# Kernel optimization log

Hardware: AMD Instinct MI355X
Metric: run time of the kernel (lower is better)

Reference implementation:

```python
import jax, jax.numpy as jnp
import numpy as np

D_MODEL = 1024
HEADS = 16
D_HEAD = D_MODEL // HEADS


def setup_inputs() -> dict:
    key = jax.random.key(0)
    ks = jax.random.split(key, 7)
    s = 1.0 / np.sqrt(D_MODEL)
    x = jax.random.normal(ks[0], (4, 2048, D_MODEL), dtype=jnp.float32)
    Wq = jax.random.uniform(ks[1], (D_MODEL, D_MODEL), jnp.float32, -s, s)
    bq = jax.random.uniform(ks[2], (D_MODEL,), jnp.float32, -s, s)
    Wk = jax.random.uniform(ks[3], (D_MODEL, D_MODEL), jnp.float32, -s, s)
    bk = jax.random.uniform(ks[4], (D_MODEL,), jnp.float32, -s, s)
    Wv = jax.random.uniform(ks[5], (D_MODEL, D_MODEL), jnp.float32, -s, s)
    bv = jax.random.uniform(ks[6], (D_MODEL,), jnp.float32, -s, s)
    return {"x": x, "Wq": Wq, "bq": bq, "Wk": Wk, "bk": bk, "Wv": Wv, "bv": bv}


def reference(x, Wq, bq, Wk, bk, Wv, bv):
    B, S, D = x.shape
    # QKV projections, split heads: [B, H, S, Dh]
    def split(t):
        return t.reshape(B, S, HEADS, D_HEAD).transpose(0, 2, 1, 3)
    q = split(x @ Wq + bq)
    k = split(x @ Wk + bk)
    v = split(x @ Wv + bv)
    scores = jnp.einsum('bhqd,bhkd->bhqk', q, k) / np.sqrt(D_HEAD).astype(jnp.float32)
    attn = jax.nn.softmax(scores, axis=-1)
    out = jnp.einsum('bhqk,bhkd->bhqd', attn, v)
    return out.transpose(0, 2, 1, 3).reshape(B, S, D)
```

## Files before the change

### kernel.cpp

```cpp
#include <hip/hip_runtime.h>

typedef _Float16 f16;
typedef __attribute__((ext_vector_type(2))) _Float16 f16x2;
typedef __attribute__((ext_vector_type(2))) __fp16   hf16x2;
typedef __attribute__((ext_vector_type(4))) _Float16 f16x4;
typedef __attribute__((ext_vector_type(8))) _Float16 f16x8;
typedef __attribute__((ext_vector_type(4))) float    f32x4;

#define D_MODEL 1024
#define HEADS   16
#define DH      64
#define SEQ     2048
#define BATCH   4
#define SSCALE  0.1803368801111204f

__device__ __forceinline__ void gload_lds16(const void* g, void* lds) {
  __builtin_amdgcn_global_load_lds(
      (const __attribute__((address_space(1))) unsigned int*)g,
      (__attribute__((address_space(3))) unsigned int*)lds, 16, 0, 0);
}

__global__ __launch_bounds__(256) void prep_kernel(const float* __restrict__ x,
                                                   const float* __restrict__ Wq,
                                                   const float* __restrict__ Wk,
                                                   const float* __restrict__ Wv,
                                                   f16* __restrict__ xb,
                                                   f16* __restrict__ wt) {
  if (blockIdx.x < 8192) {
    int i = blockIdx.x * 256 + threadIdx.x;
    float4 v = ((const float4*)x)[i];
    f16x4 h;
    h[0] = (f16)v.x; h[1] = (f16)v.y; h[2] = (f16)v.z; h[3] = (f16)v.w;
    ((f16x4*)xb)[i] = h;
    return;
  }
  int bid = blockIdx.x - 8192;
  int z = bid >> 8, rem = bid & 255;
  const float* W = z == 0 ? Wq : (z == 1 ? Wk : Wv);
  f16* out = wt + (size_t)z * D_MODEL * D_MODEL;
  __shared__ float tile[64][65];
  int n0 = (rem & 15) * 64, k0 = (rem >> 4) * 64;
  int tx = threadIdx.x & 63, ty = threadIdx.x >> 6;
#pragma unroll
  for (int r = 0; r < 16; ++r)
    tile[ty * 16 + r][tx] = W[(size_t)(k0 + ty * 16 + r) * D_MODEL + n0 + tx];
  __syncthreads();
#pragma unroll
  for (int r = 0; r < 16; ++r)
    out[(size_t)(n0 + ty * 16 + r) * D_MODEL + k0 + tx] = (f16)tile[tx][ty * 16 + r];
}

__global__ __launch_bounds__(256, 3) void qkv_gemm_kernel(
    const f16* __restrict__ xb, const f16* __restrict__ wt_all,
    const float* __restrict__ bq, const float* __restrict__ bk, const float* __restrict__ bv,
    f16* __restrict__ qout, f16* __restrict__ kout, f16* __restrict__ vtout) {
  const int bid = blockIdx.x;
  const int j = bid & 7, t = bid >> 3;
  const int by = j * 8 + (t & 7);
  const int bx = (t >> 3) & 7;
  const int z  = t >> 6;
  const f16* wt = wt_all + (size_t)z * D_MODEL * D_MODEL;
  const float* bias = z == 0 ? bq : (z == 1 ? bk : bv);
  const int n0 = bx * 128, m0 = by * 128;

  __shared__ f16 As[3][128 * 32];
  __shared__ f16 Bs[3][128 * 32];

  const int tid = threadIdx.x;
  const int lane = tid & 63, w = tid >> 6;
  const int quad = lane >> 4, l15 = lane & 15;
  const int wm = w & 1, wn = w >> 1;

  const int pce = (quad ^ ((l15 >> 1) & 3)) * 8;
  const int aoff = wm * 2048 + l15 * 32 + pce;
  const int boff = wn * 2048 + l15 * 32 + pce;

  int srow[2], scl[2];
#pragma unroll
  for (int c = 0; c < 2; ++c) {
    int slot = (w * 2 + c) * 64 + lane;
    srow[c] = slot >> 2;
    scl[c] = (slot & 3) ^ ((srow[c] >> 1) & 3);
  }

  f32x4 acc[4][4];
#pragma unroll
  for (int i = 0; i < 4; ++i)
#pragma unroll
    for (int jj = 0; jj < 4; ++jj) acc[i][jj] = (f32x4){0.f, 0.f, 0.f, 0.f};

#pragma unroll
  for (int tt = 0; tt < 2; ++tt)
#pragma unroll
    for (int c = 0; c < 2; ++c) {
      gload_lds16(xb + (size_t)(m0 + srow[c]) * D_MODEL + tt * 32 + scl[c] * 8, &As[tt][(w * 2 + c) * 512]);
      gload_lds16(wt + (size_t)(n0 + srow[c]) * D_MODEL + tt * 32 + scl[c] * 8, &Bs[tt][(w * 2 + c) * 512]);
    }

  f16x8 aP[4], bP[4];
  int buf = 0;
  for (int it = 0; it < 32; ++it) {
    if (it == 31) { asm volatile("s_waitcnt vmcnt(0)" ::: "memory"); }
    else          { asm volatile("s_waitcnt vmcnt(4)" ::: "memory"); }
    __builtin_amdgcn_s_barrier();
    __builtin_amdgcn_sched_barrier(0);
    if (it < 30) {
      const int sb = buf ? buf - 1 : 2;
      const int kn = (it + 2) * 32;
#pragma unroll
      for (int c = 0; c < 2; ++c) {
        gload_lds16(xb + (size_t)(m0 + srow[c]) * D_MODEL + kn + scl[c] * 8, &As[sb][(w * 2 + c) * 512]);
        gload_lds16(wt + (size_t)(n0 + srow[c]) * D_MODEL + kn + scl[c] * 8, &Bs[sb][(w * 2 + c) * 512]);
      }
    }
    f16x8 aC[4], bC[4];
#pragma unroll
    for (int mt = 0; mt < 4; ++mt) aC[mt] = *(const f16x8*)(&As[buf][aoff + mt * 512]);
#pragma unroll
    for (int nt = 0; nt < 4; ++nt) bC[nt] = *(const f16x8*)(&Bs[buf][boff + nt * 512]);
    if (it) {
#pragma unroll
      for (int mt = 0; mt < 4; ++mt)
#pragma unroll
        for (int nt = 0; nt < 4; ++nt)
          acc[mt][nt] = __builtin_amdgcn_mfma_f32_16x16x32_f16(aP[mt], bP[nt], acc[mt][nt], 0, 0, 0);
    }
#pragma unroll
    for (int tt = 0; tt < 4; ++tt) { aP[tt] = aC[tt]; bP[tt] = bC[tt]; }
    buf = (buf == 2) ? 0 : buf + 1;
  }
#pragma unroll
  for (int mt = 0; mt < 4; ++mt)
#pragma unroll
    for (int nt = 0; nt < 4; ++nt)
      acc[mt][nt] = __builtin_amdgcn_mfma_f32_16x16x32_f16(aP[mt], bP[nt], acc[mt][nt], 0, 0, 0);

  const float sc = (z == 0) ? SSCALE : 1.0f;
  float bcol[4];
#pragma unroll
  for (int nt = 0; nt < 4; ++nt) bcol[nt] = bias[n0 + wn * 64 + nt * 16 + l15];

  if (z < 2) {
    f16* out = (z == 0) ? qout : kout;
#pragma unroll
    for (int mt = 0; mt < 4; ++mt) {
      int mbase = m0 + wm * 64 + mt * 16 + quad * 4;
#pragma unroll
      for (int nt = 0; nt < 4; ++nt) {
        int n = n0 + wn * 64 + nt * 16 + l15;
        int h = n >> 6, dh = n & 63;
#pragma unroll
        for (int r = 0; r < 4; ++r) {
          int m = mbase + r;
          int b = m >> 11, s = m & 2047;
          out[((size_t)(b * HEADS + h) * SEQ + s) * DH + dh] = (f16)((acc[mt][nt][r] + bcol[nt]) * sc);
        }
      }
    }
  } else {
#pragma unroll
    for (int mt = 0; mt < 4; ++mt) {
      int mbase = m0 + wm * 64 + mt * 16 + quad * 4;
      int b = mbase >> 11, seq = mbase & 2047;
      int kt = seq >> 6;
#pragma unroll
      for (int nt = 0; nt < 4; ++nt) {
        int n = n0 + wn * 64 + nt * 16 + l15;
        int h = n >> 6, dh = n & 63;
        f16x4 v;
#pragma unroll
        for (int r = 0; r < 4; ++r) v[r] = (f16)(acc[mt][nt][r] + bcol[nt]);
        int phys = (quad * 2 + (mt >> 1)) ^ (dh & 7);
        size_t off = (((size_t)(b * HEADS + h) * 32 + kt) * 4096) + dh * 64 + phys * 8 + (mt & 1) * 4;
        *(f16x4*)(vtout + off) = v;
      }
    }
  }
}

__global__ __launch_bounds__(256, 2) void attn_kernel(
    const f16* __restrict__ q, const f16* __restrict__ k, const f16* __restrict__ vt,
    float* __restrict__ out, int bh0) {
  const int bh = blockIdx.x + bh0;
  const int s0 = blockIdx.y * 256;
  const int b = bh >> 4, h = bh & 15;
  const int tid = threadIdx.x, lane = tid & 63, w = tid >> 6;
  const int quad = lane >> 4, l15 = lane & 15;

  __shared__ f16 Ks[2][64 * 64];
  __shared__ f16 Vs[2][64 * 64];

  const f16* qbase = q + ((size_t)bh * SEQ + s0 + w * 64) * DH;
  const f16* kbase = k + (size_t)bh * SEQ * DH;
  const f16* vbase = vt + (size_t)bh * DH * SEQ;

  f16x8 qf[4][2];
#pragma unroll
  for (int qt = 0; qt < 4; ++qt)
#pragma unroll
    for (int ks = 0; ks < 2; ++ks)
      qf[qt][ks] = *(const f16x8*)(qbase + (qt * 16 + l15) * DH + ks * 32 + quad * 8);

  int koff[2];
  koff[0] = l15 * 64 + ((quad ^ (l15 & 7)) * 8);
  koff[1] = l15 * 64 + (((4 + quad) ^ (l15 & 7)) * 8);
  int voff2[2];
  voff2[0] = l15 * 64 + (((quad * 2) ^ (l15 & 7)) * 8);
  voff2[1] = l15 * 64 + (((quad * 2 + 1) ^ (l15 & 7)) * 8);

  int srow[2], scl[2];
#pragma unroll
  for (int c = 0; c < 2; ++c) {
    int slot = (w * 2 + c) * 64 + lane;
    srow[c] = slot >> 3;
    scl[c] = (slot & 7) ^ (srow[c] & 7);
  }
  const int vslot = ((w * 2) * 64 + lane) * 8;
  const int vslot2 = ((w * 2 + 1) * 64 + lane) * 8;

  f32x4 lsum4[4];
#pragma unroll
  for (int qt = 0; qt < 4; ++qt) lsum4[qt] = (f32x4){0.f, 0.f, 0.f, 0.f};
  f32x4 o[4][4];
#pragma unroll
  for (int i = 0; i < 4; ++i)
#pragma unroll
    for (int jj = 0; jj < 4; ++jj) o[i][jj] = (f32x4){0.f, 0.f, 0.f, 0.f};
  const f32x4 Zero = (f32x4){0.f, 0.f, 0.f, 0.f};

#pragma unroll
  for (int c = 0; c < 2; ++c)
    gload_lds16(kbase + (size_t)srow[c] * DH + scl[c] * 8, &Ks[0][(w * 2 + c) * 512]);
  gload_lds16(vbase + vslot,  &Vs[0][(w * 2) * 512]);
  gload_lds16(vbase + vslot2, &Vs[0][(w * 2 + 1) * 512]);

  for (int kt = 0; kt < SEQ / 64; ++kt) {
    const int buf = kt & 1;
    __syncthreads();
    if (kt < SEQ / 64 - 1) {
      const int kn = (kt + 1) * 64;
#pragma unroll
      for (int c = 0; c < 2; ++c)
        gload_lds16(kbase + (size_t)(kn + srow[c]) * DH + scl[c] * 8, &Ks[buf ^ 1][(w * 2 + c) * 512]);
      gload_lds16(vbase + (kt + 1) * 4096 + vslot,  &Vs[buf ^ 1][(w * 2) * 512]);
      gload_lds16(vbase + (kt + 1) * 4096 + vslot2, &Vs[buf ^ 1][(w * 2 + 1) * 512]);
    }

    f32x4 st[4][4];
#pragma unroll
    for (int mt = 0; mt < 4; ++mt) {
      f16x8 af0 = *(const f16x8*)(&Ks[buf][koff[0] + mt * 1024]);
      f16x8 af1 = *(const f16x8*)(&Ks[buf][koff[1] + mt * 1024]);
#pragma unroll
      for (int qt = 0; qt < 4; ++qt) {
        st[mt][qt] = __builtin_amdgcn_mfma_f32_16x16x32_f16(af0, qf[qt][0], Zero, 0, 0, 0);
        st[mt][qt] = __builtin_amdgcn_mfma_f32_16x16x32_f16(af1, qf[qt][1], st[mt][qt], 0, 0, 0);
      }
    }

    f16x4 pb[4][4];
#pragma unroll
    for (int ks = 0; ks < 4; ++ks)
#pragma unroll
      for (int qt = 0; qt < 4; ++qt) {
        float e0 = __builtin_amdgcn_exp2f(st[ks][qt][0]);
        float e1 = __builtin_amdgcn_exp2f(st[ks][qt][1]);
        float e2 = __builtin_amdgcn_exp2f(st[ks][qt][2]);
        float e3 = __builtin_amdgcn_exp2f(st[ks][qt][3]);
        f32x4 ev = (f32x4){e0, e1, e2, e3};
        lsum4[qt] += ev;
        f16x2 p01 = __builtin_bit_cast(f16x2, __builtin_amdgcn_cvt_pkrtz(e0, e1));
        f16x2 p23 = __builtin_bit_cast(f16x2, __builtin_amdgcn_cvt_pkrtz(e2, e3));
        pb[ks][qt] = __builtin_shufflevector(p01, p23, 0, 1, 2, 3);
      }

#pragma unroll
    for (int half = 0; half < 2; ++half)
#pragma unroll
      for (int mt = 0; mt < 4; ++mt) {
        f16x8 v8 = *(const f16x8*)(&Vs[buf][voff2[half] + mt * 1024]);
        f16x4 vaA = __builtin_shufflevector(v8, v8, 0, 1, 2, 3);
        f16x4 vaB = __builtin_shufflevector(v8, v8, 4, 5, 6, 7);
#pragma unroll
        for (int qt = 0; qt < 4; ++qt) {
          o[mt][qt] = __builtin_amdgcn_mfma_f32_16x16x16f16(vaA, pb[half * 2][qt], o[mt][qt], 0, 0, 0);
          o[mt][qt] = __builtin_amdgcn_mfma_f32_16x16x16f16(vaB, pb[half * 2 + 1][qt], o[mt][qt], 0, 0, 0);
        }
      }
  }

#pragma unroll
  for (int qt = 0; qt < 4; ++qt) {
    float l = (lsum4[qt][0] + lsum4[qt][1]) + (lsum4[qt][2] + lsum4[qt][3]);
    l += __shfl_xor(l, 16, 64);
    l += __shfl_xor(l, 32, 64);
    float inv = 1.f / l;
    int sq = s0 + w * 64 + qt * 16 + l15;
    float* obase = out + ((size_t)b * SEQ + sq) * D_MODEL + h * DH;
#pragma unroll
    for (int mt = 0; mt < 4; ++mt) {
      f32x4 vv;
#pragma unroll
      for (int r = 0; r < 4; ++r) vv[r] = o[mt][qt][r] * inv;
      *(f32x4*)(obase + mt * 16 + quad * 4) = vv;
    }
  }
}

extern "C" void kernel_launch(void* const* d_in, const int* in_sizes, int n_in,
                              void* d_out, int out_size, void* d_ws, size_t ws_size,
                              hipStream_t stream) {
  const float* x  = (const float*)d_in[0];
  const float* Wq = (const float*)d_in[1];
  const float* bq = (const float*)d_in[2];
  const float* Wk = (const float*)d_in[3];
  const float* bk = (const float*)d_in[4];
  const float* Wv = (const float*)d_in[5];
  const float* bv = (const float*)d_in[6];
  float* out = (float*)d_out;

  char* ws = (char*)d_ws;
  f16* xb = (f16*)ws;
  f16* wt = (f16*)(ws + (size_t)16 * 1024 * 1024);
  f16* q  = (f16*)(ws + (size_t)22 * 1024 * 1024);
  f16* kk = q + (size_t)BATCH * SEQ * D_MODEL;
  f16* vt = kk + (size_t)BATCH * SEQ * D_MODEL;

  prep_kernel<<<8192 + 768, 256, 0, stream>>>(x, Wq, Wk, Wv, xb, wt);
  qkv_gemm_kernel<<<1536, 256, 0, stream>>>(xb, wt, bq, bk, bv, q, kk, vt);
  attn_kernel<<<dim3(32, 8), 256, 0, stream>>>(q, kk, vt, out, 0);
  attn_kernel<<<dim3(32, 8), 256, 0, stream>>>(q, kk, vt, out, 32);
}
```

Before: 264.5 us.

## Triple-buffer K/V tiles in attention with explicit vmcnt waits and merge launches

Switches the attention kernel's K/V staging from double to triple buffering, prefetching two tiles ahead. It replaces the generic __syncthreads with explicit s_waitcnt vmcnt counts plus a raw barrier, so the newest prefetch can stay in flight. The two half-grid attention launches are merged into a single launch. The trade is more LDS per block and fragile hand-managed counter waits.

```diff
diff --git a/kernel.cpp b/kernel.cpp
--- a/kernel.cpp
+++ b/kernel.cpp
@@ -180,15 +180,15 @@
 
 __global__ __launch_bounds__(256, 2) void attn_kernel(
     const f16* __restrict__ q, const f16* __restrict__ k, const f16* __restrict__ vt,
-    float* __restrict__ out, int bh0) {
-  const int bh = blockIdx.x + bh0;
+    float* __restrict__ out) {
+  const int bh = blockIdx.x;
   const int s0 = blockIdx.y * 256;
   const int b = bh >> 4, h = bh & 15;
   const int tid = threadIdx.x, lane = tid & 63, w = tid >> 6;
   const int quad = lane >> 4, l15 = lane & 15;
 
-  __shared__ f16 Ks[2][64 * 64];
-  __shared__ f16 Vs[2][64 * 64];
+  __shared__ f16 Ks[3][64 * 64];
+  __shared__ f16 Vs[3][64 * 64];
 
   const f16* qbase = q + ((size_t)bh * SEQ + s0 + w * 64) * DH;
   const f16* kbase = k + (size_t)bh * SEQ * DH;
@@ -229,21 +229,28 @@
   const f32x4 Zero = (f32x4){0.f, 0.f, 0.f, 0.f};
 
 #pragma unroll
-  for (int c = 0; c < 2; ++c)
-    gload_lds16(kbase + (size_t)srow[c] * DH + scl[c] * 8, &Ks[0][(w * 2 + c) * 512]);
-  gload_lds16(vbase + vslot,  &Vs[0][(w * 2) * 512]);
-  gload_lds16(vbase + vslot2, &Vs[0][(w * 2 + 1) * 512]);
-
+  for (int t = 0; t < 2; ++t) {
+#pragma unroll
+    for (int c = 0; c < 2; ++c)
+      gload_lds16(kbase + (size_t)(t * 64 + srow[c]) * DH + scl[c] * 8, &Ks[t][(w * 2 + c) * 512]);
+    gload_lds16(vbase + t * 4096 + vslot,  &Vs[t][(w * 2) * 512]);
+    gload_lds16(vbase + t * 4096 + vslot2, &Vs[t][(w * 2 + 1) * 512]);
+  }
+
+  int buf = 0;
   for (int kt = 0; kt < SEQ / 64; ++kt) {
-    const int buf = kt & 1;
-    __syncthreads();
-    if (kt < SEQ / 64 - 1) {
-      const int kn = (kt + 1) * 64;
+    if (kt == SEQ / 64 - 1) { asm volatile("s_waitcnt vmcnt(0)" ::: "memory"); }
+    else                    { asm volatile("s_waitcnt vmcnt(4)" ::: "memory"); }
+    __builtin_amdgcn_s_barrier();
+    __builtin_amdgcn_sched_barrier(0);
+    if (kt < SEQ / 64 - 2) {
+      const int sb = buf ? buf - 1 : 2;
+      const int kn = (kt + 2) * 64;
 #pragma unroll
       for (int c = 0; c < 2; ++c)
-        gload_lds16(kbase + (size_t)(kn + srow[c]) * DH + scl[c] * 8, &Ks[buf ^ 1][(w * 2 + c) * 512]);
-      gload_lds16(vbase + (kt + 1) * 4096 + vslot,  &Vs[buf ^ 1][(w * 2) * 512]);
-      gload_lds16(vbase + (kt + 1) * 4096 + vslot2, &Vs[buf ^ 1][(w * 2 + 1) * 512]);
+        gload_lds16(kbase + (size_t)(kn + srow[c]) * DH + scl[c] * 8, &Ks[sb][(w * 2 + c) * 512]);
+      gload_lds16(vbase + (kt + 2) * 4096 + vslot,  &Vs[sb][(w * 2) * 512]);
+      gload_lds16(vbase + (kt + 2) * 4096 + vslot2, &Vs[sb][(w * 2 + 1) * 512]);
     }
 
     f32x4 st[4][4];
@@ -287,6 +294,7 @@
           o[mt][qt] = __builtin_amdgcn_mfma_f32_16x16x16f16(vaB, pb[half * 2 + 1][qt], o[mt][qt], 0, 0, 0);
         }
       }
+    buf = (buf == 2) ? 0 : buf + 1;
   }
 
 #pragma unroll
@@ -328,6 +336,5 @@
 
   prep_kernel<<<8192 + 768, 256, 0, stream>>>(x, Wq, Wk, Wv, xb, wt);
   qkv_gemm_kernel<<<1536, 256, 0, stream>>>(xb, wt, bq, bk, bv, q, kk, vt);
-  attn_kernel<<<dim3(32, 8), 256, 0, stream>>>(q, kk, vt, out, 0);
-  attn_kernel<<<dim3(32, 8), 256, 0, stream>>>(q, kk, vt, out, 32);
-}
+  attn_kernel<<<dim3(64, 8), 256, 0, stream>>>(q, kk, vt, out);
+}
```

Measured after the change: 245.8 us. 7.1% less time.

## Fuse fp32-to-fp16 conversion of x into QKV GEMM A-tile loads; merge attention launches

Applied to the files above, without the earlier changes.

The separate pass that converted x to fp16 is removed. The QKV GEMM now loads fp32 x rows into registers, converts them and stores the A tiles to LDS itself, with the register staging double-buffered one iteration ahead. This saves the write and re-read of a 16 MB intermediate and one large block range in the prep kernel. In exchange, the GEMM reads x in fp32 three times (once per Q/K/V tile), uses more registers and VGPR-to-LDS stores, and waits on lgkmcnt every iteration. The two attention launches are also merged into one grid of 64x8.

```diff
diff --git a/kernel.cpp b/kernel.cpp
--- a/kernel.cpp
+++ b/kernel.cpp
@@ -20,21 +20,11 @@
       (__attribute__((address_space(3))) unsigned int*)lds, 16, 0, 0);
 }
 
-__global__ __launch_bounds__(256) void prep_kernel(const float* __restrict__ x,
-                                                   const float* __restrict__ Wq,
+__global__ __launch_bounds__(256) void prep_kernel(const float* __restrict__ Wq,
                                                    const float* __restrict__ Wk,
                                                    const float* __restrict__ Wv,
-                                                   f16* __restrict__ xb,
                                                    f16* __restrict__ wt) {
-  if (blockIdx.x < 8192) {
-    int i = blockIdx.x * 256 + threadIdx.x;
-    float4 v = ((const float4*)x)[i];
-    f16x4 h;
-    h[0] = (f16)v.x; h[1] = (f16)v.y; h[2] = (f16)v.z; h[3] = (f16)v.w;
-    ((f16x4*)xb)[i] = h;
-    return;
-  }
-  int bid = blockIdx.x - 8192;
+  int bid = blockIdx.x;
   int z = bid >> 8, rem = bid & 255;
   const float* W = z == 0 ? Wq : (z == 1 ? Wk : Wv);
   f16* out = wt + (size_t)z * D_MODEL * D_MODEL;
@@ -51,7 +41,7 @@
 }
 
 __global__ __launch_bounds__(256, 3) void qkv_gemm_kernel(
-    const f16* __restrict__ xb, const f16* __restrict__ wt_all,
+    const float* __restrict__ x, const f16* __restrict__ wt_all,
     const float* __restrict__ bq, const float* __restrict__ bk, const float* __restrict__ bv,
     f16* __restrict__ qout, f16* __restrict__ kout, f16* __restrict__ vtout) {
   const int bid = blockIdx.x;
@@ -89,28 +79,64 @@
 #pragma unroll
     for (int jj = 0; jj < 4; ++jj) acc[i][jj] = (f32x4){0.f, 0.f, 0.f, 0.f};
 
-#pragma unroll
-  for (int tt = 0; tt < 2; ++tt)
+  float4 pA[2][4];
+
+#pragma unroll
+  for (int tt = 0; tt < 2; ++tt) {
+#pragma unroll
+    for (int c = 0; c < 2; ++c)
+      gload_lds16(wt + (size_t)(n0 + srow[c]) * D_MODEL + tt * 32 + scl[c] * 8, &Bs[tt][(w * 2 + c) * 512]);
 #pragma unroll
     for (int c = 0; c < 2; ++c) {
-      gload_lds16(xb + (size_t)(m0 + srow[c]) * D_MODEL + tt * 32 + scl[c] * 8, &As[tt][(w * 2 + c) * 512]);
-      gload_lds16(wt + (size_t)(n0 + srow[c]) * D_MODEL + tt * 32 + scl[c] * 8, &Bs[tt][(w * 2 + c) * 512]);
-    }
+      const float* xrow = x + (size_t)(m0 + srow[c]) * D_MODEL + tt * 32 + scl[c] * 8;
+      pA[tt][c * 2 + 0] = ((const float4*)xrow)[0];
+      pA[tt][c * 2 + 1] = ((const float4*)xrow)[1];
+    }
+  }
+  asm volatile("s_waitcnt vmcnt(6)" ::: "memory");
+#pragma unroll
+  for (int c = 0; c < 2; ++c) {
+    f16x8 hv;
+    const float4 a = pA[0][c * 2], b2 = pA[0][c * 2 + 1];
+    hv[0] = (f16)a.x;  hv[1] = (f16)a.y;  hv[2] = (f16)a.z;  hv[3] = (f16)a.w;
+    hv[4] = (f16)b2.x; hv[5] = (f16)b2.y; hv[6] = (f16)b2.z; hv[7] = (f16)b2.w;
+    *(f16x8*)(&As[0][(w * 2 + c) * 512 + lane * 8]) = hv;
+  }
 
   f16x8 aP[4], bP[4];
   int buf = 0;
+#pragma unroll 2
   for (int it = 0; it < 32; ++it) {
-    if (it == 31) { asm volatile("s_waitcnt vmcnt(0)" ::: "memory"); }
-    else          { asm volatile("s_waitcnt vmcnt(4)" ::: "memory"); }
+    const int par = it & 1;
+    asm volatile("s_waitcnt lgkmcnt(0)" ::: "memory");
     __builtin_amdgcn_s_barrier();
     __builtin_amdgcn_sched_barrier(0);
+    const int sb = buf ? buf - 1 : 2;
+    const int wb = (buf == 2) ? 0 : buf + 1;
     if (it < 30) {
-      const int sb = buf ? buf - 1 : 2;
       const int kn = (it + 2) * 32;
 #pragma unroll
+      for (int c = 0; c < 2; ++c)
+        gload_lds16(wt + (size_t)(n0 + srow[c]) * D_MODEL + kn + scl[c] * 8, &Bs[sb][(w * 2 + c) * 512]);
+#pragma unroll
       for (int c = 0; c < 2; ++c) {
-        gload_lds16(xb + (size_t)(m0 + srow[c]) * D_MODEL + kn + scl[c] * 8, &As[sb][(w * 2 + c) * 512]);
-        gload_lds16(wt + (size_t)(n0 + srow[c]) * D_MODEL + kn + scl[c] * 8, &Bs[sb][(w * 2 + c) * 512]);
+        const float* xrow = x + (size_t)(m0 + srow[c]) * D_MODEL + kn + scl[c] * 8;
+        pA[par][c * 2 + 0] = ((const float4*)xrow)[0];
+        pA[par][c * 2 + 1] = ((const float4*)xrow)[1];
+      }
+      asm volatile("s_waitcnt vmcnt(6)" ::: "memory");
+    } else {
+      asm volatile("s_waitcnt vmcnt(0)" ::: "memory");
+    }
+    if (it < 31) {
+      const int wpar = par ^ 1;
+#pragma unroll
+      for (int c = 0; c < 2; ++c) {
+        f16x8 hv;
+        const float4 a = pA[wpar][c * 2], b2 = pA[wpar][c * 2 + 1];
+        hv[0] = (f16)a.x;  hv[1] = (f16)a.y;  hv[2] = (f16)a.z;  hv[3] = (f16)a.w;
+        hv[4] = (f16)b2.x; hv[5] = (f16)b2.y; hv[6] = (f16)b2.z; hv[7] = (f16)b2.w;
+        *(f16x8*)(&As[wb][(w * 2 + c) * 512 + lane * 8]) = hv;
       }
     }
     f16x8 aC[4], bC[4];
@@ -127,7 +153,7 @@
     }
 #pragma unroll
     for (int tt = 0; tt < 4; ++tt) { aP[tt] = aC[tt]; bP[tt] = bC[tt]; }
-    buf = (buf == 2) ? 0 : buf + 1;
+    buf = wb;
   }
 #pragma unroll
   for (int mt = 0; mt < 4; ++mt)
@@ -180,8 +206,8 @@
 
 __global__ __launch_bounds__(256, 2) void attn_kernel(
     const f16* __restrict__ q, const f16* __restrict__ k, const f16* __restrict__ vt,
-    float* __restrict__ out, int bh0) {
-  const int bh = blockIdx.x + bh0;
+    float* __restrict__ out) {
+  const int bh = blockIdx.x;
   const int s0 = blockIdx.y * 256;
   const int b = bh >> 4, h = bh & 15;
   const int tid = threadIdx.x, lane = tid & 63, w = tid >> 6;
@@ -320,14 +346,12 @@
   float* out = (float*)d_out;
 
   char* ws = (char*)d_ws;
-  f16* xb = (f16*)ws;
   f16* wt = (f16*)(ws + (size_t)16 * 1024 * 1024);
   f16* q  = (f16*)(ws + (size_t)22 * 1024 * 1024);
   f16* kk = q + (size_t)BATCH * SEQ * D_MODEL;
   f16* vt = kk + (size_t)BATCH * SEQ * D_MODEL;
 
-  prep_kernel<<<8192 + 768, 256, 0, stream>>>(x, Wq, Wk, Wv, xb, wt);
-  qkv_gemm_kernel<<<1536, 256, 0, stream>>>(xb, wt, bq, bk, bv, q, kk, vt);
-  attn_kernel<<<dim3(32, 8), 256, 0, stream>>>(q, kk, vt, out, 0);
-  attn_kernel<<<dim3(32, 8), 256, 0, stream>>>(q, kk, vt, out, 32);
-}
+  prep_kernel<<<768, 256, 0, stream>>>(Wq, Wk, Wv, wt);
+  qkv_gemm_kernel<<<1536, 256, 0, stream>>>(x, wt, bq, bk, bv, q, kk, vt);
+  attn_kernel<<<dim3(64, 8), 256, 0, stream>>>(q, kk, vt, out);
+}
```

After: 460.8 us. 74.2% more time.

## Load GEMM A operand directly to registers and merge attention launches

Applied to the files above, without the earlier changes.

The QKV GEMM no longer stages the x tile through LDS. Each wave loads its A fragments straight from global memory into double-buffered registers, one k-step ahead, while B stays in the triple-buffered LDS pipeline with adjusted vmcnt waits. This cuts LDS traffic and footprint, which may raise occupancy, at the cost of more global loads per wave and more registers. The two half-sized attention launches are also merged into one grid of 64x8 to remove a launch gap and tail.

```diff
diff --git a/kernel.cpp b/kernel.cpp
--- a/kernel.cpp
+++ b/kernel.cpp
@@ -63,7 +63,6 @@
   const float* bias = z == 0 ? bq : (z == 1 ? bk : bv);
   const int n0 = bx * 128, m0 = by * 128;
 
-  __shared__ f16 As[3][128 * 32];
   __shared__ f16 Bs[3][128 * 32];
 
   const int tid = threadIdx.x;
@@ -72,7 +71,6 @@
   const int wm = w & 1, wn = w >> 1;
 
   const int pce = (quad ^ ((l15 >> 1) & 3)) * 8;
-  const int aoff = wm * 2048 + l15 * 32 + pce;
   const int boff = wn * 2048 + l15 * 32 + pce;
 
   int srow[2], scl[2];
@@ -89,33 +87,37 @@
 #pragma unroll
     for (int jj = 0; jj < 4; ++jj) acc[i][jj] = (f32x4){0.f, 0.f, 0.f, 0.f};
 
+  const f16* arow[4];
+#pragma unroll
+  for (int mt = 0; mt < 4; ++mt)
+    arow[mt] = xb + (size_t)(m0 + wm * 64 + mt * 16 + l15) * D_MODEL + quad * 8;
+
 #pragma unroll
   for (int tt = 0; tt < 2; ++tt)
 #pragma unroll
-    for (int c = 0; c < 2; ++c) {
-      gload_lds16(xb + (size_t)(m0 + srow[c]) * D_MODEL + tt * 32 + scl[c] * 8, &As[tt][(w * 2 + c) * 512]);
+    for (int c = 0; c < 2; ++c)
       gload_lds16(wt + (size_t)(n0 + srow[c]) * D_MODEL + tt * 32 + scl[c] * 8, &Bs[tt][(w * 2 + c) * 512]);
-    }
-
-  f16x8 aP[4], bP[4];
+
+  f16x8 aR0[4], aR1[4], bP[4];
   int buf = 0;
-  for (int it = 0; it < 32; ++it) {
-    if (it == 31) { asm volatile("s_waitcnt vmcnt(0)" ::: "memory"); }
-    else          { asm volatile("s_waitcnt vmcnt(4)" ::: "memory"); }
+
+  auto body = [&](int it, f16x8 (&aIss)[4], f16x8 (&aCon)[4]) {
+    if (it == 0)       { asm volatile("s_waitcnt vmcnt(2)" ::: "memory"); }
+    else if (it == 31) { asm volatile("s_waitcnt vmcnt(0)" ::: "memory"); }
+    else               { asm volatile("s_waitcnt vmcnt(6)" ::: "memory"); }
     __builtin_amdgcn_s_barrier();
     __builtin_amdgcn_sched_barrier(0);
+#pragma unroll
+    for (int mt = 0; mt < 4; ++mt)
+      aIss[mt] = *(const f16x8*)(arow[mt] + it * 32);
     if (it < 30) {
       const int sb = buf ? buf - 1 : 2;
       const int kn = (it + 2) * 32;
 #pragma unroll
-      for (int c = 0; c < 2; ++c) {
-        gload_lds16(xb + (size_t)(m0 + srow[c]) * D_MODEL + kn + scl[c] * 8, &As[sb][(w * 2 + c) * 512]);
+      for (int c = 0; c < 2; ++c)
         gload_lds16(wt + (size_t)(n0 + srow[c]) * D_MODEL + kn + scl[c] * 8, &Bs[sb][(w * 2 + c) * 512]);
-      }
-    }
-    f16x8 aC[4], bC[4];
-#pragma unroll
-    for (int mt = 0; mt < 4; ++mt) aC[mt] = *(const f16x8*)(&As[buf][aoff + mt * 512]);
+    }
+    f16x8 bC[4];
 #pragma unroll
     for (int nt = 0; nt < 4; ++nt) bC[nt] = *(const f16x8*)(&Bs[buf][boff + nt * 512]);
     if (it) {
@@ -123,17 +125,22 @@
       for (int mt = 0; mt < 4; ++mt)
 #pragma unroll
         for (int nt = 0; nt < 4; ++nt)
-          acc[mt][nt] = __builtin_amdgcn_mfma_f32_16x16x32_f16(aP[mt], bP[nt], acc[mt][nt], 0, 0, 0);
-    }
-#pragma unroll
-    for (int tt = 0; tt < 4; ++tt) { aP[tt] = aC[tt]; bP[tt] = bC[tt]; }
+          acc[mt][nt] = __builtin_amdgcn_mfma_f32_16x16x32_f16(aCon[mt], bP[nt], acc[mt][nt], 0, 0, 0);
+    }
+#pragma unroll
+    for (int nt = 0; nt < 4; ++nt) bP[nt] = bC[nt];
     buf = (buf == 2) ? 0 : buf + 1;
+  };
+
+  for (int ih = 0; ih < 16; ++ih) {
+    body(2 * ih,     aR0, aR1);
+    body(2 * ih + 1, aR1, aR0);
   }
 #pragma unroll
   for (int mt = 0; mt < 4; ++mt)
 #pragma unroll
     for (int nt = 0; nt < 4; ++nt)
-      acc[mt][nt] = __builtin_amdgcn_mfma_f32_16x16x32_f16(aP[mt], bP[nt], acc[mt][nt], 0, 0, 0);
+      acc[mt][nt] = __builtin_amdgcn_mfma_f32_16x16x32_f16(aR1[mt], bP[nt], acc[mt][nt], 0, 0, 0);
 
   const float sc = (z == 0) ? SSCALE : 1.0f;
   float bcol[4];
@@ -180,8 +187,8 @@
 
 __global__ __launch_bounds__(256, 2) void attn_kernel(
     const f16* __restrict__ q, const f16* __restrict__ k, const f16* __restrict__ vt,
-    float* __restrict__ out, int bh0) {
-  const int bh = blockIdx.x + bh0;
+    float* __restrict__ out) {
+  const int bh = blockIdx.x;
   const int s0 = blockIdx.y * 256;
   const int b = bh >> 4, h = bh & 15;
   const int tid = threadIdx.x, lane = tid & 63, w = tid >> 6;
@@ -328,6 +335,5 @@
 
   prep_kernel<<<8192 + 768, 256, 0, stream>>>(x, Wq, Wk, Wv, xb, wt);
   qkv_gemm_kernel<<<1536, 256, 0, stream>>>(xb, wt, bq, bk, bv, q, kk, vt);
-  attn_kernel<<<dim3(32, 8), 256, 0, stream>>>(q, kk, vt, out, 0);
-  attn_kernel<<<dim3(32, 8), 256, 0, stream>>>(q, kk, vt, out, 32);
-}
+  attn_kernel<<<dim3(64, 8), 256, 0, stream>>>(q, kk, vt, out);
+}
```

Measured after the change: 276.3 us. 4.5% more time.
